# Optimization experiments

Measured on AMD Instinct MI355X. Metric: run time of the kernel, lower is better.

Reference implementation:

```python
import jax, jax.numpy as jnp
import numpy as np

GAMMA = 0.5  # triplet_loss_gamma from __init__


def setup_inputs() -> dict:
    key = jax.random.key(0)
    k1, k2, k3 = jax.random.split(key, 3)
    b, n, m = 16, 2048, 2048
    scores = jax.random.normal(k1, (b, n + 1, m + 1), dtype=jnp.float32)
    gt_matches0 = jax.random.randint(k2, (b, n), 0, m, dtype=jnp.int32)
    gt_matches1 = jax.random.randint(k3, (b, m), 0, n, dtype=jnp.int32)
    return {"gt_matches0": gt_matches0, "gt_matches1": gt_matches1, "scores": scores}


def reference(gt_matches0, gt_matches1, scores):
    b, n = gt_matches0.shape
    m = gt_matches1.shape[1]
    # -1 means "unmatched" -> dustbin index (m for rows, n for cols)
    gt0 = jnp.where(gt_matches0 == -1, m, gt_matches0)
    gt1 = jnp.where(gt_matches1 == -1, n, gt_matches1)
    gamma_pos = jnp.maximum(jnp.float32(GAMMA), 0.0)  # clamp value at the matched slot

    # ---- anchor = rows (points in cloud 0) ----
    s0 = scores[:, :n, :]                                   # (b, n, m+1)
    pos0 = jnp.take_along_axis(s0, gt0[:, :, None], axis=2)  # (b, n, 1)
    # original computes -log(exp(pos)) - (-log(exp(neg))) + gamma == neg - pos + gamma
    gap0 = jnp.maximum(s0 - pos0 + GAMMA, 0.0)              # (b, n, m+1)
    # torch version excludes the matched column; its contribution is clamp(gamma, 0)
    sum0 = jnp.sum(gap0, axis=2) - gamma_pos                # (b, n)
    loss_mean = jnp.mean(2.0 * jnp.log(sum0 + 1.0), axis=1)  # (b,)

    # ---- anchor = columns (points in cloud 1) ----
    s1 = scores[:, :, :m]                                   # (b, n+1, m)
    pos1 = jnp.take_along_axis(s1, gt1[:, None, :], axis=1)  # (b, 1, m)
    gap1 = jnp.maximum(s1 - pos1 + GAMMA, 0.0)              # (b, n+1, m)
    sum1 = jnp.sum(gap1, axis=1) - gamma_pos                # (b, m)
    loss_mean2 = jnp.mean(2.0 * jnp.log(sum1 + 1.0), axis=1)  # (b,)

    return (loss_mean + loss_mean2) / 2.0
```

## Files before the change

kernel.cpp:

```cpp
#include <hip/hip_runtime.h>
#include <math.h>

#define BATCH 16
#define NN 2048
#define MM 2048
#define WW 2049
#define GAMMA 0.5f
#define NBX 64


__global__ __launch_bounds__(256) void gather_kernel(
    const float* __restrict__ scores, const int* __restrict__ gt0,
    const int* __restrict__ gt1, float* __restrict__ q0, float* __restrict__ q1)
{
    int id = blockIdx.x * 256 + threadIdx.x;
    const int half = BATCH * NN;
    if (id < half) {
        int b = id >> 11, i = id & (NN - 1);
        int g = gt0[id];
        g = (g == -1) ? MM : g;
        g = min(max(g, 0), MM);
        q0[id] = scores[(size_t)b * WW * WW + (size_t)i * WW + g] - GAMMA;
    } else {
        int id2 = id - half;
        int b = id2 >> 11, j = id2 & (MM - 1);
        int g = gt1[id2];
        g = (g == -1) ? NN : g;
        g = min(max(g, 0), NN);
        q1[id2] = scores[(size_t)b * WW * WW + (size_t)g * WW + j] - GAMMA;
    }
}

__global__ __launch_bounds__(256) void main_kernel(
    const float* __restrict__ scores, const float* __restrict__ q0,
    const float* __restrict__ q1, float* __restrict__ colpart,
    float* __restrict__ rowpart)
{
    const int b = blockIdx.y;
    const int row0 = blockIdx.x * 32;
    const int nrows = (blockIdx.x == 63) ? 33 : 32;
    const int tid = threadIdx.x;
    const int wave = tid >> 6;
    const int lane = tid & 63;

    const float* sb = scores + (size_t)b * WW * WW;
    const float* q1b = q1 + b * MM;

    float q1v[32];
    float colacc[32];
#pragma unroll
    for (int k = 0; k < 32; ++k) {
        q1v[k] = q1b[lane + 64 * k];
        colacc[k] = 0.0f;
    }

    float rowterm = 0.0f;
    for (int r = wave; r < nrows; r += 4) {
        const int i = row0 + r;
        const bool has_row = (i < NN);
        const float q0i = has_row ? q0[b * NN + i] : 0.0f;
        const float* rowp = sb + (size_t)i * WW;

        float rp = 0.0f;
#pragma unroll
        for (int k = 0; k < 32; ++k) {
            const float s = rowp[lane + 64 * k];
            rp += fmaxf(s, q0i);
            colacc[k] = fmaxf(s, q1v[k]) + colacc[k];
        }
        if (has_row) {
            if (lane == 0)
                rp += fmaxf(rowp[2048], q0i);
#pragma unroll
            for (int off = 32; off; off >>= 1)
                rp += __shfl_xor(rp, off);
            if (lane == 0)
                rowterm += 2.0f * logf(rp - 2049.0f * q0i + 0.5f);
        }
    }

    __shared__ float cl[4][MM];
    __shared__ float rw[4];
#pragma unroll
    for (int k = 0; k < 32; ++k)
        cl[wave][lane + 64 * k] = colacc[k];
    if (lane == 0) rw[wave] = rowterm;
    __syncthreads();

    float* dst = colpart + ((size_t)blockIdx.x * BATCH + b) * MM;
    for (int j = tid; j < MM; j += 256)
        dst[j] = cl[0][j] + cl[1][j] + cl[2][j] + cl[3][j];
    if (tid == 0)
        rowpart[blockIdx.x * BATCH + b] = rw[0] + rw[1] + rw[2] + rw[3];
}

__global__ __launch_bounds__(256) void reduce_cols_kernel(
    const float* __restrict__ colpart, const float* __restrict__ q1,
    float* __restrict__ colterm)
{
    const int b = blockIdx.y;
    const int j = blockIdx.x * 256 + threadIdx.x;
    const int tid = threadIdx.x;
    const int wave = tid >> 6;
    const int lane = tid & 63;

    float s0 = 0.0f, s1 = 0.0f, s2 = 0.0f, s3 = 0.0f;
#pragma unroll
    for (int bx = 0; bx < NBX; bx += 4) {
        s0 += colpart[((size_t)(bx + 0) * BATCH + b) * MM + j];
        s1 += colpart[((size_t)(bx + 1) * BATCH + b) * MM + j];
        s2 += colpart[((size_t)(bx + 2) * BATCH + b) * MM + j];
        s3 += colpart[((size_t)(bx + 3) * BATCH + b) * MM + j];
    }
    const float cs = (s0 + s1) + (s2 + s3);
    float term = 2.0f * logf(cs - 2049.0f * q1[b * MM + j] + 0.5f);

#pragma unroll
    for (int off = 32; off; off >>= 1)
        term += __shfl_xor(term, off);

    __shared__ float red[4];
    if (lane == 0) red[wave] = term;
    __syncthreads();
    if (tid == 0)
        colterm[b * 8 + blockIdx.x] = red[0] + red[1] + red[2] + red[3];
}

__global__ __launch_bounds__(64) void final_kernel(
    const float* __restrict__ rowpart, const float* __restrict__ colterm,
    float* __restrict__ out)
{
    const int b = blockIdx.x;
    const int lane = threadIdx.x;

    float rs = rowpart[lane * BATCH + b];
    float cs = (lane < 8) ? colterm[b * 8 + lane] : 0.0f;
#pragma unroll
    for (int off = 32; off; off >>= 1) {
        rs += __shfl_xor(rs, off);
        cs += __shfl_xor(cs, off);
    }
    if (lane == 0)
        out[b] = 0.5f * (rs * (1.0f / NN) + cs * (1.0f / MM));
}

extern "C" void kernel_launch(void* const* d_in, const int* in_sizes, int n_in,
                              void* d_out, int out_size, void* d_ws, size_t ws_size,
                              hipStream_t stream) {
    const int* gt0 = (const int*)d_in[0];
    const int* gt1 = (const int*)d_in[1];
    const float* scores = (const float*)d_in[2];
    float* out = (float*)d_out;

    float* ws = (float*)d_ws;
    float* q0      = ws;
    float* q1      = q0 + (size_t)BATCH * NN;
    float* colpart = q1 + (size_t)BATCH * MM;
    float* rowpart = colpart + (size_t)NBX * BATCH * MM;
    float* colterm = rowpart + (size_t)NBX * BATCH;

    gather_kernel<<<(2 * BATCH * NN) / 256, 256, 0, stream>>>(scores, gt0, gt1, q0, q1);

    dim3 grid(NBX, BATCH);
    main_kernel<<<grid, 256, 0, stream>>>(scores, q0, q1, colpart, rowpart);

    dim3 rgrid(8, BATCH);
    reduce_cols_kernel<<<rgrid, 256, 0, stream>>>(colpart, q1, colterm);

    final_kernel<<<BATCH, 64, 0, stream>>>(rowpart, colterm, out);
}
```

Before: 386.7 us.

## Split main kernel by columns per wave with more row blocks

The main kernel now assigns each wave a 512-column strip, and all four waves walk the same 16 rows together, where before each wave took whole rows. Row partial sums are combined through a small shared array, and each wave writes its column accumulators straight to global memory. This removes the 32 KB shared-memory column reduction and cuts per-thread registers from 64 to 16 accumulators. The grid doubles to 128 row blocks, which adds parallelism but also doubles the column-partial traffic read back by the reduction kernel.

New measurement: 385.9 us. Within noise of the previous version (-0.2%).

```diff
diff --git a/kernel.cpp b/kernel.cpp
--- a/kernel.cpp
+++ b/kernel.cpp
@@ -6,7 +6,8 @@
 #define MM 2048
 #define WW 2049
 #define GAMMA 0.5f
-#define NBX 64
+#define RPB 16
+#define NBX 128
 
 
 __global__ __launch_bounds__(256) void gather_kernel(
@@ -37,61 +38,69 @@
     float* __restrict__ rowpart)
 {
     const int b = blockIdx.y;
-    const int row0 = blockIdx.x * 32;
-    const int nrows = (blockIdx.x == 63) ? 33 : 32;
+    const int bx = blockIdx.x;
+    const int row0 = bx * RPB;
+    const int nrows = (bx == NBX - 1) ? (RPB + 1) : RPB;
     const int tid = threadIdx.x;
     const int wave = tid >> 6;
     const int lane = tid & 63;
+    const int col0 = 512 * wave + lane;
 
     const float* sb = scores + (size_t)b * WW * WW;
+    const float* q0b = q0 + b * NN;
     const float* q1b = q1 + b * MM;
 
-    float q1v[32];
-    float colacc[32];
+    float q1v[8], colacc[8];
 #pragma unroll
-    for (int k = 0; k < 32; ++k) {
-        q1v[k] = q1b[lane + 64 * k];
-        colacc[k] = 0.0f;
+    for (int k = 0; k < 8; ++k) { q1v[k] = q1b[col0 + 64 * k]; colacc[k] = 0.0f; }
+
+    __shared__ float part[4][RPB + 1];
+
+    const float* rowp = sb + (size_t)row0 * WW + col0;
+    for (int r = 0; r < nrows; ++r) {
+        const int i = row0 + r;
+        const bool has_row = (i < NN);
+        const float q0i = has_row ? q0b[i] : 0.0f;
+
+        float s[8];
+#pragma unroll
+        for (int k = 0; k < 8; ++k) s[k] = rowp[64 * k];
+
+        float t = 0.0f;
+#pragma unroll
+        for (int k = 0; k < 8; ++k) {
+            t += fmaxf(s[k], q0i);
+            colacc[k] += fmaxf(s[k], q1v[k]);
+        }
+        if (wave == 0 && lane == 0)
+            t += fmaxf(sb[(size_t)i * WW + 2048], q0i);
+#pragma unroll
+        for (int off = 32; off; off >>= 1)
+            t += __shfl_xor(t, off);
+        if (lane == 0) part[wave][r] = t;
+        rowp += WW;
+    }
+    __syncthreads();
+
+    if (wave == 0) {
+        float term = 0.0f;
+        if (lane < nrows) {
+            const int i = row0 + lane;
+            if (i < NN) {
+                const float rs = part[0][lane] + part[1][lane]
+                               + part[2][lane] + part[3][lane];
+                term = 2.0f * logf(rs - 2049.0f * q0b[i] + 0.5f);
+            }
+        }
+#pragma unroll
+        for (int off = 32; off; off >>= 1)
+            term += __shfl_xor(term, off);
+        if (lane == 0) rowpart[bx * BATCH + b] = term;
     }
 
-    float rowterm = 0.0f;
-    for (int r = wave; r < nrows; r += 4) {
-        const int i = row0 + r;
-        const bool has_row = (i < NN);
-        const float q0i = has_row ? q0[b * NN + i] : 0.0f;
-        const float* rowp = sb + (size_t)i * WW;
-
-        float rp = 0.0f;
+    float* dst = colpart + ((size_t)bx * BATCH + b) * MM + col0;
 #pragma unroll
-        for (int k = 0; k < 32; ++k) {
-            const float s = rowp[lane + 64 * k];
-            rp += fmaxf(s, q0i);
-            colacc[k] = fmaxf(s, q1v[k]) + colacc[k];
-        }
-        if (has_row) {
-            if (lane == 0)
-                rp += fmaxf(rowp[2048], q0i);
-#pragma unroll
-            for (int off = 32; off; off >>= 1)
-                rp += __shfl_xor(rp, off);
-            if (lane == 0)
-                rowterm += 2.0f * logf(rp - 2049.0f * q0i + 0.5f);
-        }
-    }
-
-    __shared__ float cl[4][MM];
-    __shared__ float rw[4];
-#pragma unroll
-    for (int k = 0; k < 32; ++k)
-        cl[wave][lane + 64 * k] = colacc[k];
-    if (lane == 0) rw[wave] = rowterm;
-    __syncthreads();
-
-    float* dst = colpart + ((size_t)blockIdx.x * BATCH + b) * MM;
-    for (int j = tid; j < MM; j += 256)
-        dst[j] = cl[0][j] + cl[1][j] + cl[2][j] + cl[3][j];
-    if (tid == 0)
-        rowpart[blockIdx.x * BATCH + b] = rw[0] + rw[1] + rw[2] + rw[3];
+    for (int k = 0; k < 8; ++k) dst[64 * k] = colacc[k];
 }
 
 __global__ __launch_bounds__(256) void reduce_cols_kernel(
@@ -105,7 +114,7 @@
     const int lane = tid & 63;
 
     float s0 = 0.0f, s1 = 0.0f, s2 = 0.0f, s3 = 0.0f;
-#pragma unroll
+#pragma unroll 8
     for (int bx = 0; bx < NBX; bx += 4) {
         s0 += colpart[((size_t)(bx + 0) * BATCH + b) * MM + j];
         s1 += colpart[((size_t)(bx + 1) * BATCH + b) * MM + j];
@@ -133,7 +142,7 @@
     const int b = blockIdx.x;
     const int lane = threadIdx.x;
 
-    float rs = rowpart[lane * BATCH + b];
+    float rs = rowpart[lane * BATCH + b] + rowpart[(lane + 64) * BATCH + b];
     float cs = (lane < 8) ? colterm[b * 8 + lane] : 0.0f;
 #pragma unroll
     for (int off = 32; off; off >>= 1) {
```
